# Kernel optimization log

Hardware: AMD Instinct MI355X
Metric: run time of the kernel (lower is better)

Reference implementation:

```python
import jax, jax.numpy as jnp
from jax import lax
import numpy as np

B, N, CF = 16, 4096, 64
NPOINT, NSAMPLE = 1024, 32
MLP = (64, 64, 128)
IN_CH = CF + 3
EPS = 1e-5


def _fps(xyz, npoint):
    # Farthest point sampling; deterministic start at index 0 (original uses a random start).
    Bn = xyz.shape[0]
    d0 = jnp.full(xyz.shape[:2], 1e10, xyz.dtype)
    f0 = jnp.zeros((Bn,), jnp.int32)
    def step(carry, _):
        dist, far = carry
        c = jnp.take_along_axis(xyz, far[:, None, None], axis=1)  # (B,1,3)
        d = jnp.sum((xyz - c) ** 2, axis=-1)                      # (B,N)
        dist = jnp.minimum(dist, d)
        return (dist, jnp.argmax(dist, axis=1).astype(jnp.int32)), far
    _, idxs = lax.scan(step, (d0, f0), None, length=npoint)
    return jnp.transpose(idxs)  # (B, npoint)


def _gather(pts, idx):
    # pts (B,N,C), idx (B,...) int -> (B,...,C)
    return jax.vmap(lambda p, i: p[i])(pts, idx)


def _bn_relu(x, g, b, axes):
    # training-mode batch norm (batch statistics), channel axis = 1
    m = jnp.mean(x, axes, keepdims=True)
    v = jnp.var(x, axes, keepdims=True)
    sh = (1, -1) + (1,) * (x.ndim - 2)
    return jax.nn.relu((x - m) * lax.rsqrt(v + EPS) * g.reshape(sh) + b.reshape(sh))


def _forward(xyz, points, density, params):
    fps_idx = _fps(xyz, NPOINT)
    new_xyz = _gather(xyz, fps_idx)  # (B,S,3)
    # source query_ball_point sorts distances and keeps the nsample nearest -> kNN
    d = (jnp.sum(new_xyz ** 2, -1)[:, :, None] + jnp.sum(xyz ** 2, -1)[:, None, :]
         - 2.0 * jnp.einsum('bsc,bnc->bsn', new_xyz, xyz))  # (B,S,N)
    _, idx = lax.top_k(-d, NSAMPLE)  # (B,S,ns) nearest neighbors
    gxyz = _gather(xyz, idx) - new_xyz[:, :, None, :]           # (B,S,ns,3)
    gpts = _gather(jnp.transpose(points, (0, 2, 1)), idx)       # (B,S,ns,CF)
    x = jnp.transpose(jnp.concatenate([gxyz, gpts], -1), (0, 3, 1, 2))  # (B,IN_CH,S,ns)
    (w0, b0, g0, be0, w1, b1, g1, be1, w2, b2, g2, be2, wd, bd, gd, bed) = params
    for w, b, g, be in ((w0, b0, g0, be0), (w1, b1, g1, be1), (w2, b2, g2, be2)):
        x = _bn_relu(jnp.einsum('oc,bcsk->bosk', w, x) + b[None, :, None, None], g, be, (0, 2, 3))
    # density weighting at sampled centers
    dcen = jnp.transpose(_gather(jnp.transpose(density, (0, 2, 1)), fps_idx), (0, 2, 1))  # (B,1,S)
    dw = _bn_relu(jnp.einsum('oc,bcs->bos', wd, dcen) + bd[None, :, None], gd, bed, (0, 2))  # (B,Cout,S)
    x = x * dw[..., None]
    return new_xyz, jnp.max(x, axis=-1)  # (B,S,3), (B,Cout,S)


def setup_inputs() -> dict:
    key = jax.random.key(0)
    ks = jax.random.split(key, 3)
    inp = {
        'xyz': jax.random.normal(ks[0], (B, N, 3), jnp.float32),
        'points': jax.random.normal(ks[1], (B, CF, N), jnp.float32),
        'density': jax.random.uniform(ks[2], (B, 1, N), jnp.float32),
    }
    chans = (IN_CH,) + MLP
    for i in range(3):
        cin, cout = chans[i], chans[i + 1]
        inp[f'w{i}'] = jax.random.normal(jax.random.fold_in(key, 10 + i), (cout, cin), jnp.float32) / np.sqrt(cin).astype(np.float32)
        inp[f'b{i}'] = jnp.zeros((cout,), jnp.float32)
        inp[f'g{i}'] = jnp.ones((cout,), jnp.float32)
        inp[f'be{i}'] = jnp.zeros((cout,), jnp.float32)
    inp['wd'] = jax.random.normal(jax.random.fold_in(key, 20), (MLP[-1], 1), jnp.float32)
    inp['bd'] = jnp.zeros((MLP[-1],), jnp.float32)
    inp['gd'] = jnp.ones((MLP[-1],), jnp.float32)
    inp['bed'] = jnp.zeros((MLP[-1],), jnp.float32)
    return inp


def reference(xyz, points, density, w0, b0, g0, be0, w1, b1, g1, be1, w2, b2, g2, be2, wd, bd, gd, bed):
    return _forward(xyz, points, density,
                    (w0, b0, g0, be0, w1, b1, g1, be1, w2, b2, g2, be2, wd, bd, gd, bed))
```

## Files before the change

kernel.cpp:

```cpp
#include <hip/hip_runtime.h>
#include <hip/hip_bf16.h>
#include <stdint.h>

#define NB 16
#define NN 4096
#define NCF 64
#define NS 1024
#define NK 32
#define NPTS (NB*NS*NK)
#define CIN 67
#define EPSV 1e-5f

static __device__ __forceinline__ float fmul(float a, float b){ return __fmul_rn(a,b); }
static __device__ __forceinline__ float fadd(float a, float b){ return __fadd_rn(a,b); }
static __device__ __forceinline__ float fsub(float a, float b){ return __fsub_rn(a,b); }

typedef float f2 __attribute__((ext_vector_type(2)));
#define PK_ADD(d,a,b) asm("v_pk_add_f32 %0, %1, %2" : "=v"(d) : "v"(a), "v"(b))
#define PK_MUL(d,a,b) asm("v_pk_mul_f32 %0, %1, %2" : "=v"(d) : "v"(a), "v"(b))
#define PK_FMA(d,a,b) asm("v_pk_fma_f32 %0, %1, %2, %0" : "+v"(d) : "v"(a), "v"(b))
static __device__ __forceinline__ f2 pk_add(f2 a, f2 b){ f2 d; PK_ADD(d,a,b); return d; }
static __device__ __forceinline__ f2 pk_mul(f2 a, f2 b){ f2 d; PK_MUL(d,a,b); return d; }

static __device__ __forceinline__ unsigned short f2b(float f){
  unsigned u = __float_as_uint(f);
  return (unsigned short)((u + 0x7FFFu + ((u>>16)&1u)) >> 16);
}

static __device__ __forceinline__ unsigned long long umax64(unsigned long long a,
                                                            unsigned long long b){
  return a > b ? a : b;
}

template<int CTRL>
static __device__ __forceinline__ float dppmax_f32(float x){
  float o = __uint_as_float((unsigned)__builtin_amdgcn_update_dpp(
      0, (int)__float_as_uint(x), CTRL, 0xf, 0xf, true));
  return fmaxf(x, o);
}
static __device__ __forceinline__ float wave_max63_f32(float x){
  x = dppmax_f32<0x111>(x);
  x = dppmax_f32<0x112>(x);
  x = dppmax_f32<0x114>(x);
  x = dppmax_f32<0x118>(x);
  x = dppmax_f32<0x142>(x);
  x = dppmax_f32<0x143>(x);
  return x;
}
static __device__ __forceinline__ float group8_max_f32(float x){
  x = dppmax_f32<0xB1>(x);
  x = dppmax_f32<0x4E>(x);
  x = dppmax_f32<0x141>(x);
  return x;
}
template<int CTRL>
static __device__ __forceinline__ f2 dppadd_f2(f2 x){
  f2 o;
  o.x = __uint_as_float((unsigned)__builtin_amdgcn_update_dpp(
      0, (int)__float_as_uint(x.x), CTRL, 0xf, 0xf, true));
  o.y = __uint_as_float((unsigned)__builtin_amdgcn_update_dpp(
      0, (int)__float_as_uint(x.y), CTRL, 0xf, 0xf, true));
  return pk_add(x, o);
}
static __device__ __forceinline__ f2 wave_sum63_f2(f2 x){
  x = dppadd_f2<0x111>(x);
  x = dppadd_f2<0x112>(x);
  x = dppadd_f2<0x114>(x);
  x = dppadd_f2<0x118>(x);
  x = dppadd_f2<0x142>(x);
  x = dppadd_f2<0x143>(x);
  return x;
}
static __device__ __forceinline__ f2 half_sum31_f2(f2 x){
  x = dppadd_f2<0x111>(x);
  x = dppadd_f2<0x112>(x);
  x = dppadd_f2<0x114>(x);
  x = dppadd_f2<0x118>(x);
  x = dppadd_f2<0x142>(x);
  return x;
}
static __device__ __forceinline__ unsigned long long readlane_u64(unsigned long long v, int l){
  unsigned lo = (unsigned)__builtin_amdgcn_readlane((int)(unsigned)v, l);
  unsigned hi = (unsigned)__builtin_amdgcn_readlane((int)(unsigned)(v>>32), l);
  return ((unsigned long long)hi<<32) | lo;
}
static __device__ __forceinline__ unsigned long long wave_shr1_u64(unsigned long long x){
  unsigned lo = (unsigned)__builtin_amdgcn_update_dpp(
      0, (int)(unsigned)x, 0x138, 0xf, 0xf, true);
  unsigned hi = (unsigned)__builtin_amdgcn_update_dpp(
      0, (int)(unsigned)(x>>32), 0x138, 0xf, 0xf, true);
  return ((unsigned long long)hi<<32) | lo;
}

__global__ __launch_bounds__(256) void prep_kernel(const float* __restrict__ pts,
    const float* __restrict__ xyz, float* __restrict__ ptsT, float* __restrict__ sqx){
  int blk = blockIdx.x;
  int b = blk >> 4;
  int n = ((blk & 15) << 8) + threadIdx.x;
  const float* src = pts + (size_t)b*NCF*NN + n;
  float v[NCF];
  #pragma unroll
  for (int c=0;c<NCF;c++) v[c] = src[(size_t)c*NN];
  float4* dst = (float4*)(ptsT + ((size_t)b*NN + n)*NCF);
  #pragma unroll
  for (int j=0;j<16;j++) dst[j] = make_float4(v[4*j],v[4*j+1],v[4*j+2],v[4*j+3]);
  const float* xp = xyz + ((size_t)b*NN + n)*3;
  float x=xp[0], y=xp[1], z=xp[2];
  sqx[(size_t)b*NN+n] = fadd(fadd(fmul(x,x),fmul(y,y)),fmul(z,z));
}

#define FT 512
__global__ __launch_bounds__(FT) void fps_kernel(const float* __restrict__ xyz,
    int* __restrict__ fidx, float* __restrict__ newxyz){
  int b = blockIdx.x;
  __shared__ float4 s4[NN];
  __shared__ unsigned long long candK[2][8];
  const int tid = threadIdx.x;
  const int lane = tid & 63;
  const int wv = tid >> 6;
  for (int i = tid; i < NN; i += FT){
    const float* p = xyz + ((size_t)b*NN + i)*3;
    s4[i] = make_float4(p[0], p[1], p[2], 0.f);
  }
  __syncthreads();
  f2 px[4], py[4], pz[4], d2[4];
  #pragma unroll
  for (int m=0;m<4;m++){
    float4 a = s4[tid*8 + 2*m];
    float4 c = s4[tid*8 + 2*m + 1];
    px[m] = (f2){a.x, c.x};
    py[m] = (f2){a.y, c.y};
    pz[m] = (f2){a.z, c.z};
    d2[m] = (f2){1e10f, 1e10f};
  }
  int far = 0;
  float4 cc = s4[0];
  for (int s=0;s<NS;s++){
    if (tid==0){
      fidx[b*NS+s] = far;
      float* o = newxyz + ((size_t)b*NS+s)*3;
      o[0]=cc.x; o[1]=cc.y; o[2]=cc.z;
    }
    f2 ncx = (f2){-cc.x,-cc.x}, ncy = (f2){-cc.y,-cc.y}, ncz = (f2){-cc.z,-cc.z};
    float bv = -1.0f; int bj = 0;
    #pragma unroll
    for (int m=0;m<4;m++){
      f2 dx,dy,dz,xx,yy,zz,ss,dd;
      PK_ADD(dx, px[m], ncx);
      PK_ADD(dy, py[m], ncy);
      PK_ADD(dz, pz[m], ncz);
      PK_MUL(xx, dx, dx);
      PK_MUL(yy, dy, dy);
      PK_ADD(ss, xx, yy);
      PK_MUL(zz, dz, dz);
      PK_ADD(dd, ss, zz);
      float u0 = fminf(d2[m].x, dd.x);
      float u1 = fminf(d2[m].y, dd.y);
      d2[m].x = u0; d2[m].y = u1;
      if (u0 > bv){ bv = u0; bj = 2*m; }
      if (u1 > bv){ bv = u1; bj = 2*m+1; }
    }
    int nbest = (tid<<3) + bj;
    float mv = wave_max63_f32(bv);
    float mvu = __uint_as_float((unsigned)__builtin_amdgcn_readlane(
        (int)__float_as_uint(mv), 63));
    unsigned long long tiedm = __ballot(bv == mvu);
    int wl = __ffsll(tiedm) - 1;
    unsigned nwin = (unsigned)__builtin_amdgcn_readlane(nbest, wl);
    if (lane == 0)
      candK[s&1][wv] = ((unsigned long long)__float_as_uint(mvu) << 32)
                     | (unsigned long long)(unsigned)~nwin;
    __syncthreads();
    const ulonglong2* cp = (const ulonglong2*)candK[s&1];
    ulonglong2 c0=cp[0], c1=cp[1], c2=cp[2], c3=cp[3];
    unsigned long long kk = umax64(
        umax64(umax64(c0.x,c0.y), umax64(c1.x,c1.y)),
        umax64(umax64(c2.x,c2.y), umax64(c3.x,c3.y)));
    far = (int)(~(unsigned)kk) & (NN-1);
    cc = s4[far];
  }
}

__global__ __launch_bounds__(256) void dcen_kernel(const float* __restrict__ density,
    const int* __restrict__ fidx, float* __restrict__ dcen){
  int i = blockIdx.x*256 + threadIdx.x;
  int b = i >> 10;
  dcen[i] = density[(size_t)b*NN + fidx[i]];
}

__global__ __launch_bounds__(256) void dstats_kernel(const float* __restrict__ dcen,
    float* __restrict__ dstat){
  float s=0.f, q=0.f;
  for (int i=threadIdx.x; i<NB*NS; i+=256){ float v=dcen[i]; s+=v; q+=v*v; }
  __shared__ float ls[256], lq[256];
  ls[threadIdx.x]=s; lq[threadIdx.x]=q;
  __syncthreads();
  for (int off=128; off>0; off>>=1){
    if (threadIdx.x<off){ ls[threadIdx.x]+=ls[threadIdx.x+off]; lq[threadIdx.x]+=lq[threadIdx.x+off]; }
    __syncthreads();
  }
  if (threadIdx.x==0){
    float m = ls[0]/(float)(NB*NS);
    dstat[0]=m; dstat[1]=lq[0]/(float)(NB*NS) - m*m;
  }
}

__global__ __launch_bounds__(256) void knn_kernel(const float* __restrict__ xyz,
    const float* __restrict__ sqx, const float* __restrict__ newxyz,
    int* __restrict__ kidx){
  const int lane = threadIdx.x & 63;
  const int g = blockIdx.x*4 + (threadIdx.x >> 6);
  const int b = g >> 10;
  const float* cp = newxyz + (size_t)g*3;
  const float cx=cp[0], cy=cp[1], cz=cp[2];
  const float sqc = fadd(fadd(fmul(cx,cx),fmul(cy,cy)),fmul(cz,cz));
  const float* xb  = xyz + (size_t)b*NN*3;
  const float* sqb = sqx + (size_t)b*NN;
  unsigned long long kept  = ~0ULL;
  unsigned long long worst = ~0ULL;
  for (int n0=0; n0<NN; n0+=64){
    const int n = n0 + lane;
    const float* xp = xb + (size_t)n*3;
    float x=xp[0], y=xp[1], z=xp[2];
    float dot = fadd(fadd(fmul(cx,x),fmul(cy,y)),fmul(cz,z));
    float d = fsub(fadd(sqc, sqb[n]), fmul(2.0f,dot));
    unsigned u = __float_as_uint(d);
    u = (u & 0x80000000u) ? ~u : (u | 0x80000000u);
    unsigned long long ck = ((unsigned long long)u << 32) | (unsigned)n;
    unsigned long long mask = __ballot(ck < worst);
    while (mask){
      const int l = __ffsll(mask) - 1;
      mask &= mask - 1;
      const unsigned long long k = readlane_u64(ck, l);
      if (k < worst){
        bool m = kept > k;
        unsigned long long M = __ballot(m) << 1;
        unsigned long long sh = wave_shr1_u64(kept);
        bool msh = (M >> lane) & 1ULL;
        unsigned long long ins = msh ? sh : k;
        kept = m ? ins : kept;
        worst = readlane_u64(kept, 31);
      }
    }
  }
  if (lane < 32) kidx[(size_t)g*NK + lane] = (int)(kept & 0xFFFFFFFFULL);
}

__global__ __launch_bounds__(256) void conv1_kernel(const float* __restrict__ xyz,
    const float* __restrict__ ptsT, const float* __restrict__ newxyz,
    const int* __restrict__ kidx, const float* __restrict__ w0,
    const float* __restrict__ b0, unsigned short* __restrict__ z1,
    float* __restrict__ partial){
  __shared__ float si[CIN][128];
  __shared__ float sw[CIN][64];
  __shared__ float sbias[64];
  const int tid = threadIdx.x;
  for (int i = tid; i < CIN*64; i += 256){
    int o = i / CIN, c = i - o*CIN;
    sw[c][o] = w0[i];
  }
  if (tid < 64) sbias[tid] = b0[tid];
  const int p0 = blockIdx.x * 128;
  if (tid < 128){
    const int p = p0 + tid;
    const int g = p >> 5;
    const int b = g >> 10;
    const int n = kidx[p];
    const float* xp = xyz + ((size_t)b*NN + n)*3;
    const float* cp = newxyz + (size_t)g*3;
    si[0][tid] = xp[0]-cp[0];
    si[1][tid] = xp[1]-cp[1];
    si[2][tid] = xp[2]-cp[2];
    const float4* pr = (const float4*)(ptsT + ((size_t)b*NN + n)*NCF);
    #pragma unroll
    for (int j=0;j<16;j++){
      float4 v = pr[j];
      si[3+4*j][tid]=v.x; si[4+4*j][tid]=v.y; si[5+4*j][tid]=v.z; si[6+4*j][tid]=v.w;
    }
  }
  __syncthreads();
  const int og = tid >> 6;
  const int pg = tid & 63;
  f2 acc0[8], acc1[8];
  const f2* bp = (const f2*)&sbias[og*16];
  #pragma unroll
  for (int q=0;q<8;q++){ f2 bb = bp[q]; acc0[q]=bb; acc1[q]=bb; }
  for (int c=0;c<CIN;c++){
    float2 a = *(const float2*)&si[c][2*pg];
    const f2* wr = (const f2*)&sw[c][og*16];
    f2 a0 = (f2){a.x, a.x};
    f2 a1 = (f2){a.y, a.y};
    #pragma unroll
    for (int q=0;q<8;q++){
      f2 w = wr[q];
      PK_FMA(acc0[q], a0, w);
      PK_FMA(acc1[q], a1, w);
    }
  }
  unsigned v[8];
  #pragma unroll
  for (int j=0;j<8;j++) v[j] = (unsigned)f2b(acc0[j].x) | ((unsigned)f2b(acc0[j].y)<<16);
  uint4* d0 = (uint4*)(z1 + (size_t)(p0+2*pg)*64 + og*16);
  d0[0]=make_uint4(v[0],v[1],v[2],v[3]); d0[1]=make_uint4(v[4],v[5],v[6],v[7]);
  #pragma unroll
  for (int j=0;j<8;j++) v[j] = (unsigned)f2b(acc1[j].x) | ((unsigned)f2b(acc1[j].y)<<16);
  uint4* d1 = (uint4*)(z1 + (size_t)(p0+2*pg+1)*64 + og*16);
  d1[0]=make_uint4(v[0],v[1],v[2],v[3]); d1[1]=make_uint4(v[4],v[5],v[6],v[7]);
  #pragma unroll
  for (int q=0;q<8;q++){
    f2 s = pk_add(acc0[q], acc1[q]);
    f2 sq = pk_add(pk_mul(acc0[q],acc0[q]), pk_mul(acc1[q],acc1[q]));
    s = wave_sum63_f2(s);
    sq = wave_sum63_f2(sq);
    if (pg==63){
      float* pb = partial + (size_t)blockIdx.x*128 + og*16;
      pb[2*q]=s.x; pb[2*q+1]=s.y;
      pb[64+2*q]=sq.x; pb[64+2*q+1]=sq.y;
    }
  }
}

__global__ __launch_bounds__(256) void conv2_kernel(const unsigned short* __restrict__ z1,
    const float* __restrict__ w1, const float* __restrict__ b1,
    const float* __restrict__ scale1, const float* __restrict__ shift1,
    unsigned short* __restrict__ z2, float* __restrict__ partial){
  __shared__ float si[64][128];
  __shared__ float sw[64][64];
  __shared__ float sbias[64];
  const int tid = threadIdx.x;
  for (int i = tid; i < 64*64; i += 256){
    int o = i >> 6, c = i & 63;
    sw[c][o] = w1[i];
  }
  if (tid < 64) sbias[tid] = b1[tid];
  const int p0 = blockIdx.x * 128;
  if (tid < 128){
    const uint4* zr = (const uint4*)(z1 + (size_t)(p0 + tid)*64);
    #pragma unroll
    for (int j=0;j<8;j++){
      uint4 vv = zr[j];
      unsigned a[4] = {vv.x, vv.y, vv.z, vv.w};
      #pragma unroll
      for (int t=0;t<4;t++){
        int c = j*8 + t*2;
        float lo = __uint_as_float(a[t] << 16);
        float hi = __uint_as_float(a[t] & 0xFFFF0000u);
        si[c][tid]   = fmaxf(lo*scale1[c]   + shift1[c],   0.0f);
        si[c+1][tid] = fmaxf(hi*scale1[c+1] + shift1[c+1], 0.0f);
      }
    }
  }
  __syncthreads();
  const int og = tid >> 6;
  const int pg = tid & 63;
  f2 acc0[8], acc1[8];
  const f2* bp = (const f2*)&sbias[og*16];
  #pragma unroll
  for (int q=0;q<8;q++){ f2 bb = bp[q]; acc0[q]=bb; acc1[q]=bb; }
  for (int c=0;c<64;c++){
    float2 a = *(const float2*)&si[c][2*pg];
    const f2* wr = (const f2*)&sw[c][og*16];
    f2 a0 = (f2){a.x, a.x};
    f2 a1 = (f2){a.y, a.y};
    #pragma unroll
    for (int q=0;q<8;q++){
      f2 w = wr[q];
      PK_FMA(acc0[q], a0, w);
      PK_FMA(acc1[q], a1, w);
    }
  }
  unsigned v[8];
  #pragma unroll
  for (int j=0;j<8;j++) v[j] = (unsigned)f2b(acc0[j].x) | ((unsigned)f2b(acc0[j].y)<<16);
  uint4* d0 = (uint4*)(z2 + (size_t)(p0+2*pg)*64 + og*16);
  d0[0]=make_uint4(v[0],v[1],v[2],v[3]); d0[1]=make_uint4(v[4],v[5],v[6],v[7]);
  #pragma unroll
  for (int j=0;j<8;j++) v[j] = (unsigned)f2b(acc1[j].x) | ((unsigned)f2b(acc1[j].y)<<16);
  uint4* d1 = (uint4*)(z2 + (size_t)(p0+2*pg+1)*64 + og*16);
  d1[0]=make_uint4(v[0],v[1],v[2],v[3]); d1[1]=make_uint4(v[4],v[5],v[6],v[7]);
  #pragma unroll
  for (int q=0;q<8;q++){
    f2 s = pk_add(acc0[q], acc1[q]);
    f2 sq = pk_add(pk_mul(acc0[q],acc0[q]), pk_mul(acc1[q],acc1[q]));
    s = wave_sum63_f2(s);
    sq = wave_sum63_f2(sq);
    if (pg==63){
      float* pb = partial + (size_t)blockIdx.x*128 + og*16;
      pb[2*q]=s.x; pb[2*q+1]=s.y;
      pb[64+2*q]=sq.x; pb[64+2*q+1]=sq.y;
    }
  }
}

__global__ __launch_bounds__(256) void conv3_kernel(const unsigned short* __restrict__ z2,
    const float* __restrict__ w2, const float* __restrict__ b2,
    const float* __restrict__ scale2, const float* __restrict__ shift2,
    float* __restrict__ m3, float* __restrict__ partial){
  __shared__ float si[64][128];
  __shared__ float sw[64][128];
  const int tid = threadIdx.x;
  for (int i = tid; i < 64*128; i += 256){
    int o = i >> 6, c = i & 63;
    sw[c][o] = w2[i];
  }
  const int p0 = blockIdx.x * 128;
  if (tid < 128){
    const uint4* zr = (const uint4*)(z2 + (size_t)(p0 + tid)*64);
    #pragma unroll
    for (int j=0;j<8;j++){
      uint4 vv = zr[j];
      unsigned a[4]={vv.x,vv.y,vv.z,vv.w};
      #pragma unroll
      for (int t=0;t<4;t++){
        int c = j*8+t*2;
        float lo=__uint_as_float(a[t]<<16), hi=__uint_as_float(a[t]&0xFFFF0000u);
        si[c][tid]   = fmaxf(lo*scale2[c]+shift2[c],0.f);
        si[c+1][tid] = fmaxf(hi*scale2[c+1]+shift2[c+1],0.f);
      }
    }
  }
  __syncthreads();
  const int og = tid >> 5;
  const int pg = tid & 31;
  f2 acc[4][8];
  const f2* bq = (const f2*)(b2 + og*16);
  #pragma unroll
  for (int q=0;q<8;q++){
    f2 bb = bq[q];
    #pragma unroll
    for (int p=0;p<4;p++) acc[p][q]=bb;
  }
  for (int c=0;c<64;c++){
    float4 a = *(const float4*)&si[c][pg*4];
    const f2* wr = (const f2*)&sw[c][og*16];
    f2 a0=(f2){a.x,a.x}, a1=(f2){a.y,a.y}, a2=(f2){a.z,a.z}, a3=(f2){a.w,a.w};
    #pragma unroll
    for (int q=0;q<8;q++){
      f2 w = wr[q];
      PK_FMA(acc[0][q], a0, w);
      PK_FMA(acc[1][q], a1, w);
      PK_FMA(acc[2][q], a2, w);
      PK_FMA(acc[3][q], a3, w);
    }
  }
  float mx[16];
  #pragma unroll
  for (int q=0;q<8;q++){
    float mxx = fmaxf(fmaxf(acc[0][q].x,acc[1][q].x), fmaxf(acc[2][q].x,acc[3][q].x));
    float mxy = fmaxf(fmaxf(acc[0][q].y,acc[1][q].y), fmaxf(acc[2][q].y,acc[3][q].y));
    mx[2*q]   = group8_max_f32(mxx);
    mx[2*q+1] = group8_max_f32(mxy);
  }
  if ((pg & 7)==0){
    const int center = blockIdx.x*4 + (pg>>3);
    float4* mp = (float4*)(m3 + (size_t)center*128 + og*16);
    #pragma unroll
    for (int q=0;q<4;q++) mp[q] = make_float4(mx[4*q],mx[4*q+1],mx[4*q+2],mx[4*q+3]);
  }
  #pragma unroll
  for (int q=0;q<8;q++){
    f2 s = pk_add(pk_add(acc[0][q],acc[1][q]), pk_add(acc[2][q],acc[3][q]));
    f2 sq = pk_add(pk_add(pk_mul(acc[0][q],acc[0][q]), pk_mul(acc[1][q],acc[1][q])),
                   pk_add(pk_mul(acc[2][q],acc[2][q]), pk_mul(acc[3][q],acc[3][q])));
    s = half_sum31_f2(s);
    sq = half_sum31_f2(sq);
    if (pg==31){
      float* pb = partial + (size_t)blockIdx.x*256 + og*16;
      pb[2*q]=s.x; pb[2*q+1]=s.y;
      pb[128+2*q]=sq.x; pb[128+2*q+1]=sq.y;
    }
  }
}

__global__ __launch_bounds__(256) void mkbn_kernel(const float* __restrict__ partial,
    int nrows, int stride, const float* __restrict__ g, const float* __restrict__ be,
    float* __restrict__ scale, float* __restrict__ shift, float inv_count){
  const int c = blockIdx.x;
  const int C = gridDim.x;
  float s=0.f, q=0.f;
  for (int r=threadIdx.x; r<nrows; r+=256){
    s += partial[(size_t)r*stride + c];
    q += partial[(size_t)r*stride + C + c];
  }
  __shared__ float ls[256], lq[256];
  ls[threadIdx.x]=s; lq[threadIdx.x]=q;
  __syncthreads();
  for (int off=128; off>0; off>>=1){
    if (threadIdx.x < off){ ls[threadIdx.x]+=ls[threadIdx.x+off]; lq[threadIdx.x]+=lq[threadIdx.x+off]; }
    __syncthreads();
  }
  if (threadIdx.x==0){
    float mean = ls[0]*inv_count;
    float var  = lq[0]*inv_count - mean*mean;
    float sc = g[c]*rsqrtf(var + EPSV);
    scale[c]=sc; shift[c]=be[c]-mean*sc;
  }
}

__global__ __launch_bounds__(256) void final_kernel(const float* __restrict__ m3,
    const float* __restrict__ dcen, const float* __restrict__ scale3,
    const float* __restrict__ shift3, const float* __restrict__ wd,
    const float* __restrict__ bd, const float* __restrict__ gd,
    const float* __restrict__ bed, const float* __restrict__ dstat,
    float* __restrict__ out){
  size_t i = (size_t)blockIdx.x*256 + threadIdx.x;
  int s  = (int)(i & 1023);
  int ch = (int)((i >> 10) & 127);
  int b  = (int)(i >> 17);
  float mean_d = dstat[0], var_d = dstat[1];
  float w = wd[ch];
  float meanp = w*mean_d + bd[ch];
  float varp  = w*w*var_d;
  float dsc = gd[ch]*rsqrtf(varp + EPSV);
  float dsh = bed[ch] - meanp*dsc;
  float pre = w*dcen[b*NS+s] + bd[ch];
  float dw  = fmaxf(dsc*pre + dsh, 0.0f);
  float z   = m3[((size_t)(b*NS+s))*128 + ch];
  float x   = fmaxf(scale3[ch]*z + shift3[ch], 0.0f);
  out[i] = x*dw;
}

extern "C" void kernel_launch(void* const* d_in, const int* in_sizes, int n_in,
                              void* d_out, int out_size, void* d_ws, size_t ws_size,
                              hipStream_t stream){
  const float* xyz     = (const float*)d_in[0];
  const float* points  = (const float*)d_in[1];
  const float* density = (const float*)d_in[2];
  const float* w0 = (const float*)d_in[3];
  const float* b0 = (const float*)d_in[4];
  const float* g0 = (const float*)d_in[5];
  const float* be0= (const float*)d_in[6];
  const float* w1 = (const float*)d_in[7];
  const float* b1 = (const float*)d_in[8];
  const float* g1 = (const float*)d_in[9];
  const float* be1= (const float*)d_in[10];
  const float* w2 = (const float*)d_in[11];
  const float* b2 = (const float*)d_in[12];
  const float* g2 = (const float*)d_in[13];
  const float* be2= (const float*)d_in[14];
  const float* wd = (const float*)d_in[15];
  const float* bd = (const float*)d_in[16];
  const float* gd = (const float*)d_in[17];
  const float* bed= (const float*)d_in[18];

  float* out = (float*)d_out;
  float* newxyz = out;
  float* out1   = out + (size_t)NB*NS*3;

  float* ptsT = (float*)d_ws;
  float* sqx  = ptsT + (size_t)NB*NN*NCF;
  int*   fidx = (int*)(sqx + (size_t)NB*NN);
  float* dcen = (float*)(fidx + NB*NS);
  int*   kidx = (int*)(dcen + NB*NS);
  unsigned short* z1 = (unsigned short*)(kidx + NPTS);
  unsigned short* z2 = z1 + (size_t)NPTS*64;
  float* m3   = (float*)(z2 + (size_t)NPTS*64);
  float* p1   = m3 + (size_t)NB*NS*128;
  float* p2   = p1 + 4096*128;
  float* p3   = p2 + 4096*128;
  float* bnp  = p3 + 4096*256;
  float* dstat= bnp + 512;

  hipLaunchKernelGGL(prep_kernel,  dim3(256),  dim3(256), 0, stream, points, xyz, ptsT, sqx);
  hipLaunchKernelGGL(fps_kernel,   dim3(NB),   dim3(FT),  0, stream, xyz, fidx, newxyz);
  hipLaunchKernelGGL(dcen_kernel,  dim3(64),   dim3(256), 0, stream, density, fidx, dcen);
  hipLaunchKernelGGL(dstats_kernel,dim3(1),    dim3(256), 0, stream, dcen, dstat);
  hipLaunchKernelGGL(knn_kernel,   dim3(4096), dim3(256), 0, stream, xyz, sqx, newxyz, kidx);
  hipLaunchKernelGGL(conv1_kernel, dim3(4096), dim3(256), 0, stream, xyz, ptsT, newxyz, kidx, w0, b0, z1, p1);
  hipLaunchKernelGGL(mkbn_kernel,  dim3(64),   dim3(256), 0, stream, p1, 4096, 128, g0, be0, bnp+0,   bnp+64,  1.0f/(float)NPTS);
  hipLaunchKernelGGL(conv2_kernel, dim3(4096), dim3(256), 0, stream, z1, w1, b1, bnp+0, bnp+64, z2, p2);
  hipLaunchKernelGGL(mkbn_kernel,  dim3(64),   dim3(256), 0, stream, p2, 4096, 128, g1, be1, bnp+128, bnp+192, 1.0f/(float)NPTS);
  hipLaunchKernelGGL(conv3_kernel, dim3(4096), dim3(256), 0, stream, z2, w2, b2, bnp+128, bnp+192, m3, p3);
  hipLaunchKernelGGL(mkbn_kernel,  dim3(128),  dim3(256), 0, stream, p3, 4096, 256, g2, be2, bnp+256, bnp+384, 1.0f/(float)NPTS);
  hipLaunchKernelGGL(final_kernel, dim3(8192), dim3(256), 0, stream, m3, dcen, bnp+256, bnp+384, wd, bd, gd, bed, dstat, out1);
}
```

Measured before the change: 1.345 ms.

## Use bf16 MFMA for the three pointwise conv layers and store features as bf16

Replaces the packed-FP32 FMA loops in conv1, conv2 and conv3 with 16x16x32 bf16 MFMA instructions. Operands are staged in LDS as padded bf16 tiles. The transposed point features are now kept in bf16, which halves gather traffic in conv1. Batch-norm statistics and the per-center max are recomputed from the MFMA output layout with row-level DPP reductions. The cost is lower input precision (bf16 activations and weights) and extra zero-padding of the 67-channel input to 96.

Result: faster. 1.137 ms (-15.5%).

```diff
diff --git a/kernel.cpp b/kernel.cpp
--- a/kernel.cpp
+++ b/kernel.cpp
@@ -18,15 +18,18 @@
 typedef float f2 __attribute__((ext_vector_type(2)));
 #define PK_ADD(d,a,b) asm("v_pk_add_f32 %0, %1, %2" : "=v"(d) : "v"(a), "v"(b))
 #define PK_MUL(d,a,b) asm("v_pk_mul_f32 %0, %1, %2" : "=v"(d) : "v"(a), "v"(b))
-#define PK_FMA(d,a,b) asm("v_pk_fma_f32 %0, %1, %2, %0" : "+v"(d) : "v"(a), "v"(b))
 static __device__ __forceinline__ f2 pk_add(f2 a, f2 b){ f2 d; PK_ADD(d,a,b); return d; }
-static __device__ __forceinline__ f2 pk_mul(f2 a, f2 b){ f2 d; PK_MUL(d,a,b); return d; }
+
+typedef short bf16x8 __attribute__((ext_vector_type(8)));
+typedef float f32x4 __attribute__((ext_vector_type(4)));
 
 static __device__ __forceinline__ unsigned short f2b(float f){
   unsigned u = __float_as_uint(f);
   return (unsigned short)((u + 0x7FFFu + ((u>>16)&1u)) >> 16);
 }
-
+static __device__ __forceinline__ unsigned pack2(float a, float b){
+  return (unsigned)f2b(a) | ((unsigned)f2b(b)<<16);
+}
 static __device__ __forceinline__ unsigned long long umax64(unsigned long long a,
                                                             unsigned long long b){
   return a > b ? a : b;
@@ -39,18 +42,20 @@
   return fmaxf(x, o);
 }
 static __device__ __forceinline__ float wave_max63_f32(float x){
-  x = dppmax_f32<0x111>(x);
-  x = dppmax_f32<0x112>(x);
-  x = dppmax_f32<0x114>(x);
-  x = dppmax_f32<0x118>(x);
-  x = dppmax_f32<0x142>(x);
-  x = dppmax_f32<0x143>(x);
+  x = dppmax_f32<0x111>(x); x = dppmax_f32<0x112>(x);
+  x = dppmax_f32<0x114>(x); x = dppmax_f32<0x118>(x);
+  x = dppmax_f32<0x142>(x); x = dppmax_f32<0x143>(x);
   return x;
 }
-static __device__ __forceinline__ float group8_max_f32(float x){
-  x = dppmax_f32<0xB1>(x);
-  x = dppmax_f32<0x4E>(x);
-  x = dppmax_f32<0x141>(x);
+template<int CTRL>
+static __device__ __forceinline__ float dppmax_keep(float x){
+  float o = __uint_as_float((unsigned)__builtin_amdgcn_update_dpp(
+      (int)__float_as_uint(x), (int)__float_as_uint(x), CTRL, 0xf, 0xf, false));
+  return fmaxf(x, o);
+}
+static __device__ __forceinline__ float row16_max_f32(float x){
+  x = dppmax_keep<0x111>(x); x = dppmax_keep<0x112>(x);
+  x = dppmax_keep<0x114>(x); x = dppmax_keep<0x118>(x);
   return x;
 }
 template<int CTRL>
@@ -62,21 +67,9 @@
       0, (int)__float_as_uint(x.y), CTRL, 0xf, 0xf, true));
   return pk_add(x, o);
 }
-static __device__ __forceinline__ f2 wave_sum63_f2(f2 x){
-  x = dppadd_f2<0x111>(x);
-  x = dppadd_f2<0x112>(x);
-  x = dppadd_f2<0x114>(x);
-  x = dppadd_f2<0x118>(x);
-  x = dppadd_f2<0x142>(x);
-  x = dppadd_f2<0x143>(x);
-  return x;
-}
-static __device__ __forceinline__ f2 half_sum31_f2(f2 x){
-  x = dppadd_f2<0x111>(x);
-  x = dppadd_f2<0x112>(x);
-  x = dppadd_f2<0x114>(x);
-  x = dppadd_f2<0x118>(x);
-  x = dppadd_f2<0x142>(x);
+static __device__ __forceinline__ f2 row16_sum_f2(f2 x){
+  x = dppadd_f2<0x111>(x); x = dppadd_f2<0x112>(x);
+  x = dppadd_f2<0x114>(x); x = dppadd_f2<0x118>(x);
   return x;
 }
 static __device__ __forceinline__ unsigned long long readlane_u64(unsigned long long v, int l){
@@ -93,7 +86,8 @@
 }
 
 __global__ __launch_bounds__(256) void prep_kernel(const float* __restrict__ pts,
-    const float* __restrict__ xyz, float* __restrict__ ptsT, float* __restrict__ sqx){
+    const float* __restrict__ xyz, unsigned short* __restrict__ ptsT,
+    float* __restrict__ sqx){
   int blk = blockIdx.x;
   int b = blk >> 4;
   int n = ((blk & 15) << 8) + threadIdx.x;
@@ -101,9 +95,11 @@
   float v[NCF];
   #pragma unroll
   for (int c=0;c<NCF;c++) v[c] = src[(size_t)c*NN];
-  float4* dst = (float4*)(ptsT + ((size_t)b*NN + n)*NCF);
-  #pragma unroll
-  for (int j=0;j<16;j++) dst[j] = make_float4(v[4*j],v[4*j+1],v[4*j+2],v[4*j+3]);
+  uint4* dst = (uint4*)(ptsT + ((size_t)b*NN + n)*NCF);
+  #pragma unroll
+  for (int j=0;j<8;j++)
+    dst[j] = make_uint4(pack2(v[8*j],v[8*j+1]), pack2(v[8*j+2],v[8*j+3]),
+                        pack2(v[8*j+4],v[8*j+5]), pack2(v[8*j+6],v[8*j+7]));
   const float* xp = xyz + ((size_t)b*NN + n)*3;
   float x=xp[0], y=xp[1], z=xp[2];
   sqx[(size_t)b*NN+n] = fadd(fadd(fmul(x,x),fmul(y,y)),fmul(z,z));
@@ -246,76 +242,83 @@
   if (lane < 32) kidx[(size_t)g*NK + lane] = (int)(kept & 0xFFFFFFFFULL);
 }
 
+
 __global__ __launch_bounds__(256) void conv1_kernel(const float* __restrict__ xyz,
-    const float* __restrict__ ptsT, const float* __restrict__ newxyz,
+    const unsigned short* __restrict__ ptsT, const float* __restrict__ newxyz,
     const int* __restrict__ kidx, const float* __restrict__ w0,
     const float* __restrict__ b0, unsigned short* __restrict__ z1,
     float* __restrict__ partial){
-  __shared__ float si[CIN][128];
-  __shared__ float sw[CIN][64];
-  __shared__ float sbias[64];
+  __shared__ unsigned short sa[128][104];
+  __shared__ unsigned short swb[64][104];
   const int tid = threadIdx.x;
-  for (int i = tid; i < CIN*64; i += 256){
-    int o = i / CIN, c = i - o*CIN;
-    sw[c][o] = w0[i];
-  }
-  if (tid < 64) sbias[tid] = b0[tid];
   const int p0 = blockIdx.x * 128;
+  for (int i = tid; i < 64*52; i += 256){
+    int o = i / 52, pr = i - o*52, c0 = 2*pr;
+    float v0 = (c0 < 64) ? w0[o*CIN + 3 + c0] : (c0 < 67 ? w0[o*CIN + (c0-64)] : 0.f);
+    int c1 = c0 + 1;
+    float v1 = (c1 < 64) ? w0[o*CIN + 3 + c1] : (c1 < 67 ? w0[o*CIN + (c1-64)] : 0.f);
+    *(unsigned*)&swb[o][c0] = pack2(v0, v1);
+  }
+  #pragma unroll
+  for (int j=0;j<4;j++){
+    int idx = tid + j*256;
+    int pt = idx >> 3, cg = idx & 7;
+    int p = p0 + pt, g = p >> 5, b = g >> 10;
+    int n = kidx[p];
+    uint4 vv = *(const uint4*)(ptsT + ((size_t)b*NN + n)*NCF + cg*8);
+    *(uint4*)&sa[pt][cg*8] = vv;
+  }
   if (tid < 128){
-    const int p = p0 + tid;
-    const int g = p >> 5;
-    const int b = g >> 10;
-    const int n = kidx[p];
+    int p = p0 + tid, g = p >> 5, b = g >> 10;
+    int n = kidx[p];
     const float* xp = xyz + ((size_t)b*NN + n)*3;
     const float* cp = newxyz + (size_t)g*3;
-    si[0][tid] = xp[0]-cp[0];
-    si[1][tid] = xp[1]-cp[1];
-    si[2][tid] = xp[2]-cp[2];
-    const float4* pr = (const float4*)(ptsT + ((size_t)b*NN + n)*NCF);
-    #pragma unroll
-    for (int j=0;j<16;j++){
-      float4 v = pr[j];
-      si[3+4*j][tid]=v.x; si[4+4*j][tid]=v.y; si[5+4*j][tid]=v.z; si[6+4*j][tid]=v.w;
-    }
+    float gx = xp[0]-cp[0], gy = xp[1]-cp[1], gz = xp[2]-cp[2];
+    *(uint2*)&sa[tid][64] = make_uint2(pack2(gx,gy), pack2(gz,0.f));
+    *(uint2*)&sa[tid][68] = make_uint2(0u,0u);
+    uint4 zz = make_uint4(0u,0u,0u,0u);
+    *(uint4*)&sa[tid][72] = zz; *(uint4*)&sa[tid][80] = zz;
+    *(uint4*)&sa[tid][88] = zz; *(uint4*)&sa[tid][96] = zz;
   }
   __syncthreads();
-  const int og = tid >> 6;
-  const int pg = tid & 63;
-  f2 acc0[8], acc1[8];
-  const f2* bp = (const f2*)&sbias[og*16];
-  #pragma unroll
-  for (int q=0;q<8;q++){ f2 bb = bp[q]; acc0[q]=bb; acc1[q]=bb; }
-  for (int c=0;c<CIN;c++){
-    float2 a = *(const float2*)&si[c][2*pg];
-    const f2* wr = (const f2*)&sw[c][og*16];
-    f2 a0 = (f2){a.x, a.x};
-    f2 a1 = (f2){a.y, a.y};
-    #pragma unroll
-    for (int q=0;q<8;q++){
-      f2 w = wr[q];
-      PK_FMA(acc0[q], a0, w);
-      PK_FMA(acc1[q], a1, w);
-    }
-  }
-  unsigned v[8];
-  #pragma unroll
-  for (int j=0;j<8;j++) v[j] = (unsigned)f2b(acc0[j].x) | ((unsigned)f2b(acc0[j].y)<<16);
-  uint4* d0 = (uint4*)(z1 + (size_t)(p0+2*pg)*64 + og*16);
-  d0[0]=make_uint4(v[0],v[1],v[2],v[3]); d0[1]=make_uint4(v[4],v[5],v[6],v[7]);
-  #pragma unroll
-  for (int j=0;j<8;j++) v[j] = (unsigned)f2b(acc1[j].x) | ((unsigned)f2b(acc1[j].y)<<16);
-  uint4* d1 = (uint4*)(z1 + (size_t)(p0+2*pg+1)*64 + og*16);
-  d1[0]=make_uint4(v[0],v[1],v[2],v[3]); d1[1]=make_uint4(v[4],v[5],v[6],v[7]);
-  #pragma unroll
-  for (int q=0;q<8;q++){
-    f2 s = pk_add(acc0[q], acc1[q]);
-    f2 sq = pk_add(pk_mul(acc0[q],acc0[q]), pk_mul(acc1[q],acc1[q]));
-    s = wave_sum63_f2(s);
-    sq = wave_sum63_f2(sq);
-    if (pg==63){
-      float* pb = partial + (size_t)blockIdx.x*128 + og*16;
-      pb[2*q]=s.x; pb[2*q+1]=s.y;
-      pb[64+2*q]=sq.x; pb[64+2*q+1]=sq.y;
+  const int wv = tid >> 6, lane = tid & 63;
+  const int r15 = lane & 15, q = lane >> 4;
+  f32x4 acc[8];
+  #pragma unroll
+  for (int t=0;t<8;t++) acc[t] = (f32x4){0.f,0.f,0.f,0.f};
+  #pragma unroll
+  for (int ks=0; ks<3; ks++){
+    bf16x8 af = *(const bf16x8*)&swb[wv*16 + r15][ks*32 + q*8];
+    #pragma unroll
+    for (int t=0;t<8;t++){
+      bf16x8 bfr = *(const bf16x8*)&sa[t*16 + r15][ks*32 + q*8];
+      acc[t] = __builtin_amdgcn_mfma_f32_16x16x32_bf16(af, bfr, acc[t], 0,0,0);
+    }
+  }
+  float bias[4];
+  #pragma unroll
+  for (int r=0;r<4;r++) bias[r] = b0[wv*16 + q*4 + r];
+  f2 st[4];
+  #pragma unroll
+  for (int r=0;r<4;r++) st[r] = (f2){0.f,0.f};
+  #pragma unroll
+  for (int t=0;t<8;t++){
+    float z0=acc[t][0]+bias[0], z1v=acc[t][1]+bias[1];
+    float z2v=acc[t][2]+bias[2], z3v=acc[t][3]+bias[3];
+    st[0] = pk_add(st[0], (f2){z0, z0*z0});
+    st[1] = pk_add(st[1], (f2){z1v, z1v*z1v});
+    st[2] = pk_add(st[2], (f2){z2v, z2v*z2v});
+    st[3] = pk_add(st[3], (f2){z3v, z3v*z3v});
+    *(uint2*)(z1 + (size_t)(p0 + t*16 + r15)*64 + wv*16 + q*4)
+        = make_uint2(pack2(z0,z1v), pack2(z2v,z3v));
+  }
+  #pragma unroll
+  for (int r=0;r<4;r++){
+    f2 s = row16_sum_f2(st[r]);
+    if (r15 == 15){
+      int ch = wv*16 + q*4 + r;
+      partial[(size_t)blockIdx.x*128 + ch] = s.x;
+      partial[(size_t)blockIdx.x*128 + 64 + ch] = s.y;
     }
   }
 }
@@ -324,70 +327,71 @@
     const float* __restrict__ w1, const float* __restrict__ b1,
     const float* __restrict__ scale1, const float* __restrict__ shift1,
     unsigned short* __restrict__ z2, float* __restrict__ partial){
-  __shared__ float si[64][128];
-  __shared__ float sw[64][64];
-  __shared__ float sbias[64];
+  __shared__ unsigned short sa[128][72];
+  __shared__ unsigned short swb[64][72];
   const int tid = threadIdx.x;
-  for (int i = tid; i < 64*64; i += 256){
-    int o = i >> 6, c = i & 63;
-    sw[c][o] = w1[i];
-  }
-  if (tid < 64) sbias[tid] = b1[tid];
   const int p0 = blockIdx.x * 128;
-  if (tid < 128){
-    const uint4* zr = (const uint4*)(z1 + (size_t)(p0 + tid)*64);
-    #pragma unroll
-    for (int j=0;j<8;j++){
-      uint4 vv = zr[j];
-      unsigned a[4] = {vv.x, vv.y, vv.z, vv.w};
-      #pragma unroll
-      for (int t=0;t<4;t++){
-        int c = j*8 + t*2;
-        float lo = __uint_as_float(a[t] << 16);
-        float hi = __uint_as_float(a[t] & 0xFFFF0000u);
-        si[c][tid]   = fmaxf(lo*scale1[c]   + shift1[c],   0.0f);
-        si[c+1][tid] = fmaxf(hi*scale1[c+1] + shift1[c+1], 0.0f);
-      }
-    }
+  for (int i = tid; i < 64*32; i += 256){
+    int o = i >> 5, c0 = (i & 31)*2;
+    *(unsigned*)&swb[o][c0] = pack2(w1[o*64+c0], w1[o*64+c0+1]);
+  }
+  #pragma unroll
+  for (int j=0;j<4;j++){
+    int idx = tid + j*256;
+    int pt = idx >> 3, cg = idx & 7;
+    uint4 vv = *(const uint4*)(z1 + (size_t)(p0+pt)*64 + cg*8);
+    unsigned a[4] = {vv.x, vv.y, vv.z, vv.w};
+    unsigned r[4];
+    #pragma unroll
+    for (int t=0;t<4;t++){
+      int c = cg*8 + t*2;
+      float lo = __uint_as_float(a[t] << 16);
+      float hi = __uint_as_float(a[t] & 0xFFFF0000u);
+      float alo = fmaxf(lo*scale1[c]   + shift1[c],   0.f);
+      float ahi = fmaxf(hi*scale1[c+1] + shift1[c+1], 0.f);
+      r[t] = pack2(alo, ahi);
+    }
+    *(uint4*)&sa[pt][cg*8] = make_uint4(r[0],r[1],r[2],r[3]);
   }
   __syncthreads();
-  const int og = tid >> 6;
-  const int pg = tid & 63;
-  f2 acc0[8], acc1[8];
-  const f2* bp = (const f2*)&sbias[og*16];
-  #pragma unroll
-  for (int q=0;q<8;q++){ f2 bb = bp[q]; acc0[q]=bb; acc1[q]=bb; }
-  for (int c=0;c<64;c++){
-    float2 a = *(const float2*)&si[c][2*pg];
-    const f2* wr = (const f2*)&sw[c][og*16];
-    f2 a0 = (f2){a.x, a.x};
-    f2 a1 = (f2){a.y, a.y};
-    #pragma unroll
-    for (int q=0;q<8;q++){
-      f2 w = wr[q];
-      PK_FMA(acc0[q], a0, w);
-      PK_FMA(acc1[q], a1, w);
-    }
-  }
-  unsigned v[8];
-  #pragma unroll
-  for (int j=0;j<8;j++) v[j] = (unsigned)f2b(acc0[j].x) | ((unsigned)f2b(acc0[j].y)<<16);
-  uint4* d0 = (uint4*)(z2 + (size_t)(p0+2*pg)*64 + og*16);
-  d0[0]=make_uint4(v[0],v[1],v[2],v[3]); d0[1]=make_uint4(v[4],v[5],v[6],v[7]);
-  #pragma unroll
-  for (int j=0;j<8;j++) v[j] = (unsigned)f2b(acc1[j].x) | ((unsigned)f2b(acc1[j].y)<<16);
-  uint4* d1 = (uint4*)(z2 + (size_t)(p0+2*pg+1)*64 + og*16);
-  d1[0]=make_uint4(v[0],v[1],v[2],v[3]); d1[1]=make_uint4(v[4],v[5],v[6],v[7]);
-  #pragma unroll
-  for (int q=0;q<8;q++){
-    f2 s = pk_add(acc0[q], acc1[q]);
-    f2 sq = pk_add(pk_mul(acc0[q],acc0[q]), pk_mul(acc1[q],acc1[q]));
-    s = wave_sum63_f2(s);
-    sq = wave_sum63_f2(sq);
-    if (pg==63){
-      float* pb = partial + (size_t)blockIdx.x*128 + og*16;
-      pb[2*q]=s.x; pb[2*q+1]=s.y;
-      pb[64+2*q]=sq.x; pb[64+2*q+1]=sq.y;
+  const int wv = tid >> 6, lane = tid & 63;
+  const int r15 = lane & 15, q = lane >> 4;
+  f32x4 acc[8];
+  #pragma unroll
+  for (int t=0;t<8;t++) acc[t] = (f32x4){0.f,0.f,0.f,0.f};
+  #pragma unroll
+  for (int ks=0; ks<2; ks++){
+    bf16x8 af = *(const bf16x8*)&swb[wv*16 + r15][ks*32 + q*8];
+    #pragma unroll
+    for (int t=0;t<8;t++){
+      bf16x8 bfr = *(const bf16x8*)&sa[t*16 + r15][ks*32 + q*8];
+      acc[t] = __builtin_amdgcn_mfma_f32_16x16x32_bf16(af, bfr, acc[t], 0,0,0);
+    }
+  }
+  float bias[4];
+  #pragma unroll
+  for (int r=0;r<4;r++) bias[r] = b1[wv*16 + q*4 + r];
+  f2 st[4];
+  #pragma unroll
+  for (int r=0;r<4;r++) st[r] = (f2){0.f,0.f};
+  #pragma unroll
+  for (int t=0;t<8;t++){
+    float z0=acc[t][0]+bias[0], z1v=acc[t][1]+bias[1];
+    float z2v=acc[t][2]+bias[2], z3v=acc[t][3]+bias[3];
+    st[0] = pk_add(st[0], (f2){z0, z0*z0});
+    st[1] = pk_add(st[1], (f2){z1v, z1v*z1v});
+    st[2] = pk_add(st[2], (f2){z2v, z2v*z2v});
+    st[3] = pk_add(st[3], (f2){z3v, z3v*z3v});
+    *(uint2*)(z2 + (size_t)(p0 + t*16 + r15)*64 + wv*16 + q*4)
+        = make_uint2(pack2(z0,z1v), pack2(z2v,z3v));
+  }
+  #pragma unroll
+  for (int r=0;r<4;r++){
+    f2 s = row16_sum_f2(st[r]);
+    if (r15 == 15){
+      int ch = wv*16 + q*4 + r;
+      partial[(size_t)blockIdx.x*128 + ch] = s.x;
+      partial[(size_t)blockIdx.x*128 + 64 + ch] = s.y;
     }
   }
 }
@@ -396,78 +400,87 @@
     const float* __restrict__ w2, const float* __restrict__ b2,
     const float* __restrict__ scale2, const float* __restrict__ shift2,
     float* __restrict__ m3, float* __restrict__ partial){
-  __shared__ float si[64][128];
-  __shared__ float sw[64][128];
+  __shared__ unsigned short sa[128][72];
+  __shared__ unsigned short swb[128][72];
   const int tid = threadIdx.x;
-  for (int i = tid; i < 64*128; i += 256){
-    int o = i >> 6, c = i & 63;
-    sw[c][o] = w2[i];
-  }
   const int p0 = blockIdx.x * 128;
-  if (tid < 128){
-    const uint4* zr = (const uint4*)(z2 + (size_t)(p0 + tid)*64);
-    #pragma unroll
-    for (int j=0;j<8;j++){
-      uint4 vv = zr[j];
-      unsigned a[4]={vv.x,vv.y,vv.z,vv.w};
+  for (int i = tid; i < 128*32; i += 256){
+    int o = i >> 5, c0 = (i & 31)*2;
+    *(unsigned*)&swb[o][c0] = pack2(w2[o*64+c0], w2[o*64+c0+1]);
+  }
+  #pragma unroll
+  for (int j=0;j<4;j++){
+    int idx = tid + j*256;
+    int pt = idx >> 3, cg = idx & 7;
+    uint4 vv = *(const uint4*)(z2 + (size_t)(p0+pt)*64 + cg*8);
+    unsigned a[4] = {vv.x, vv.y, vv.z, vv.w};
+    unsigned r[4];
+    #pragma unroll
+    for (int t=0;t<4;t++){
+      int c = cg*8 + t*2;
+      float lo = __uint_as_float(a[t] << 16);
+      float hi = __uint_as_float(a[t] & 0xFFFF0000u);
+      float alo = fmaxf(lo*scale2[c]   + shift2[c],   0.f);
+      float ahi = fmaxf(hi*scale2[c+1] + shift2[c+1], 0.f);
+      r[t] = pack2(alo, ahi);
+    }
+    *(uint4*)&sa[pt][cg*8] = make_uint4(r[0],r[1],r[2],r[3]);
+  }
+  __syncthreads();
+  const int wv = tid >> 6, lane = tid & 63;
+  const int r15 = lane & 15, q = lane >> 4;
+  f32x4 acc[2][8];
+  #pragma unroll
+  for (int mm=0;mm<2;mm++)
+    #pragma unroll
+    for (int t=0;t<8;t++) acc[mm][t] = (f32x4){0.f,0.f,0.f,0.f};
+  #pragma unroll
+  for (int ks=0; ks<2; ks++){
+    bf16x8 af0 = *(const bf16x8*)&swb[(wv*2+0)*16 + r15][ks*32 + q*8];
+    bf16x8 af1 = *(const bf16x8*)&swb[(wv*2+1)*16 + r15][ks*32 + q*8];
+    #pragma unroll
+    for (int t=0;t<8;t++){
+      bf16x8 bfr = *(const bf16x8*)&sa[t*16 + r15][ks*32 + q*8];
+      acc[0][t] = __builtin_amdgcn_mfma_f32_16x16x32_bf16(af0, bfr, acc[0][t], 0,0,0);
+      acc[1][t] = __builtin_amdgcn_mfma_f32_16x16x32_bf16(af1, bfr, acc[1][t], 0,0,0);
+    }
+  }
+  #pragma unroll
+  for (int mm=0;mm<2;mm++){
+    const int base = (wv*2+mm)*16;
+    float bias[4];
+    #pragma unroll
+    for (int r=0;r<4;r++) bias[r] = b2[base + q*4 + r];
+    float zv[8][4];
+    f2 st[4];
+    #pragma unroll
+    for (int r=0;r<4;r++) st[r] = (f2){0.f,0.f};
+    #pragma unroll
+    for (int t=0;t<8;t++){
       #pragma unroll
-      for (int t=0;t<4;t++){
-        int c = j*8+t*2;
-        float lo=__uint_as_float(a[t]<<16), hi=__uint_as_float(a[t]&0xFFFF0000u);
-        si[c][tid]   = fmaxf(lo*scale2[c]+shift2[c],0.f);
-        si[c+1][tid] = fmaxf(hi*scale2[c+1]+shift2[c+1],0.f);
+      for (int r=0;r<4;r++){
+        float z = acc[mm][t][r] + bias[r];
+        zv[t][r] = z;
+        st[r] = pk_add(st[r], (f2){z, z*z});
       }
     }
-  }
-  __syncthreads();
-  const int og = tid >> 5;
-  const int pg = tid & 31;
-  f2 acc[4][8];
-  const f2* bq = (const f2*)(b2 + og*16);
-  #pragma unroll
-  for (int q=0;q<8;q++){
-    f2 bb = bq[q];
-    #pragma unroll
-    for (int p=0;p<4;p++) acc[p][q]=bb;
-  }
-  for (int c=0;c<64;c++){
-    float4 a = *(const float4*)&si[c][pg*4];
-    const f2* wr = (const f2*)&sw[c][og*16];
-    f2 a0=(f2){a.x,a.x}, a1=(f2){a.y,a.y}, a2=(f2){a.z,a.z}, a3=(f2){a.w,a.w};
-    #pragma unroll
-    for (int q=0;q<8;q++){
-      f2 w = wr[q];
-      PK_FMA(acc[0][q], a0, w);
-      PK_FMA(acc[1][q], a1, w);
-      PK_FMA(acc[2][q], a2, w);
-      PK_FMA(acc[3][q], a3, w);
-    }
-  }
-  float mx[16];
-  #pragma unroll
-  for (int q=0;q<8;q++){
-    float mxx = fmaxf(fmaxf(acc[0][q].x,acc[1][q].x), fmaxf(acc[2][q].x,acc[3][q].x));
-    float mxy = fmaxf(fmaxf(acc[0][q].y,acc[1][q].y), fmaxf(acc[2][q].y,acc[3][q].y));
-    mx[2*q]   = group8_max_f32(mxx);
-    mx[2*q+1] = group8_max_f32(mxy);
-  }
-  if ((pg & 7)==0){
-    const int center = blockIdx.x*4 + (pg>>3);
-    float4* mp = (float4*)(m3 + (size_t)center*128 + og*16);
-    #pragma unroll
-    for (int q=0;q<4;q++) mp[q] = make_float4(mx[4*q],mx[4*q+1],mx[4*q+2],mx[4*q+3]);
-  }
-  #pragma unroll
-  for (int q=0;q<8;q++){
-    f2 s = pk_add(pk_add(acc[0][q],acc[1][q]), pk_add(acc[2][q],acc[3][q]));
-    f2 sq = pk_add(pk_add(pk_mul(acc[0][q],acc[0][q]), pk_mul(acc[1][q],acc[1][q])),
-                   pk_add(pk_mul(acc[2][q],acc[2][q]), pk_mul(acc[3][q],acc[3][q])));
-    s = half_sum31_f2(s);
-    sq = half_sum31_f2(sq);
-    if (pg==31){
-      float* pb = partial + (size_t)blockIdx.x*256 + og*16;
-      pb[2*q]=s.x; pb[2*q+1]=s.y;
-      pb[128+2*q]=sq.x; pb[128+2*q+1]=sq.y;
+    #pragma unroll
+    for (int r=0;r<4;r++){
+      f2 s = row16_sum_f2(st[r]);
+      if (r15 == 15){
+        int ch = base + q*4 + r;
+        partial[(size_t)blockIdx.x*256 + ch] = s.x;
+        partial[(size_t)blockIdx.x*256 + 128 + ch] = s.y;
+      }
+    }
+    #pragma unroll
+    for (int c=0;c<4;c++){
+      #pragma unroll
+      for (int r=0;r<4;r++){
+        float m = row16_max_f32(fmaxf(zv[2*c][r], zv[2*c+1][r]));
+        if (r15 == 15)
+          m3[(size_t)(blockIdx.x*4 + c)*128 + base + q*4 + r] = m;
+      }
     }
   }
 }
@@ -547,8 +560,8 @@
   float* newxyz = out;
   float* out1   = out + (size_t)NB*NS*3;
 
-  float* ptsT = (float*)d_ws;
-  float* sqx  = ptsT + (size_t)NB*NN*NCF;
+  unsigned short* ptsT = (unsigned short*)d_ws;
+  float* sqx  = (float*)(ptsT + (size_t)NB*NN*NCF);
   int*   fidx = (int*)(sqx + (size_t)NB*NN);
   float* dcen = (float*)(fidx + NB*NS);
   int*   kidx = (int*)(dcen + NB*NS);
```
